# Kernel optimization log

Measured on AMD Instinct MI355X. Metric: run time of the kernel, lower is better.

The kernel has to match this reference:

```python
import jax, jax.numpy as jnp
import numpy as np

MESSAGE_PASSES = 3  # constants.message_passes
F_NODE = 64   # hidden_node_features
F_EDGE = 16   # n_edge_features
M_MSG = 64    # message_size
OUT_DIM = 128
B, N = 8, 256
EDGE_DENSITY = 0.1


def setup_inputs() -> dict:
    key = jax.random.key(0)
    ks = jax.random.split(key, 12)
    nodes = jax.random.normal(ks[0], (B, N, F_NODE), dtype=jnp.float32)
    # sparse positive edge features: rand * bernoulli connectivity (avg degree ~ N*density)
    raw = jax.random.uniform(ks[1], (B, N, N, F_EDGE), dtype=jnp.float32)
    conn = (jax.random.uniform(ks[2], (B, N, N)) < EDGE_DENSITY).astype(jnp.float32)
    edges = raw * conn[..., None]
    s = 0.05
    return {
        "nodes": nodes,
        "edges": edges,
        # message MLP: cat(neighbour, edge) -> message_size
        "W_msg": jax.random.normal(ks[3], (F_NODE + F_EDGE, M_MSG), dtype=jnp.float32) * s,
        "b_msg": jnp.zeros((M_MSG,), dtype=jnp.float32),
        # GRU cell (input=message_size, hidden=F_NODE), gates [r|z|n]
        "W_i": jax.random.normal(ks[4], (M_MSG, 3 * F_NODE), dtype=jnp.float32) * s,
        "W_h": jax.random.normal(ks[5], (F_NODE, 3 * F_NODE), dtype=jnp.float32) * s,
        "b_i": jnp.zeros((3 * F_NODE,), dtype=jnp.float32),
        "b_h": jnp.zeros((3 * F_NODE,), dtype=jnp.float32),
        # gated readout
        "W_g": jax.random.normal(ks[6], (2 * F_NODE, OUT_DIM), dtype=jnp.float32) * s,
        "b_g": jnp.zeros((OUT_DIM,), dtype=jnp.float32),
        "W_e": jax.random.normal(ks[7], (F_NODE, OUT_DIM), dtype=jnp.float32) * s,
        "b_e": jnp.zeros((OUT_DIM,), dtype=jnp.float32),
    }


def reference(nodes, edges, W_msg, b_msg, W_i, W_h, b_i, b_h, W_g, b_g, W_e, b_e):
    # adjacency[b,i,j] != 0  <=>  edge (i<-j) exists (original: edges.sum(3).nonzero)
    adjacency = edges.sum(axis=-1)                                   # (B,N,N)
    nbr_mask = (adjacency != 0).astype(nodes.dtype)                  # (B,N,N)
    node_mask = (adjacency.sum(axis=-1) != 0)                        # (B,N) bool
    node_mask_f = node_mask.astype(nodes.dtype)

    h = nodes                                                        # hidden_nodes init = nodes
    b, n, f = nodes.shape
    for _ in range(MESSAGE_PASSES):
        # message_terms over all (node i, neighbour j) pairs; masked sum == padded-gather sum
        nghb = jnp.broadcast_to(h[:, None, :, :], (b, n, n, f))      # (B,N,N,F) neighbour feats
        feat = jnp.concatenate([nghb, edges], axis=-1)               # (B,N,N,F+E)
        terms = jax.nn.relu(feat @ W_msg + b_msg)                    # (B,N,N,M)
        messages = jnp.einsum('bijm,bij->bim', terms, nbr_mask)      # summation aggregation
        # GRU cell update
        gi = messages @ W_i + b_i                                    # (B,N,3F)
        gh = h @ W_h + b_h
        ir, iz, inn = jnp.split(gi, 3, axis=-1)
        hr, hz, hn = jnp.split(gh, 3, axis=-1)
        r = jax.nn.sigmoid(ir + hr)
        z = jax.nn.sigmoid(iz + hz)
        ng = jnp.tanh(inn + r * hn)
        h_new = (1.0 - z) * ng + z * h
        # only nodes with nonzero degree are scattered back (original indexes node_batch idc)
        h = jnp.where(node_mask[..., None], h_new, h)

    # gated readout: sum_i mask_i * sigmoid(g([h_i, x_i])) * e(h_i)
    gate = jax.nn.sigmoid(jnp.concatenate([h, nodes], axis=-1) @ W_g + b_g)  # (B,N,OUT)
    emb = h @ W_e + b_e                                                      # (B,N,OUT)
    out = jnp.einsum('bno,bn->bo', gate * emb, node_mask_f)                  # (B,OUT)
    return out
```

## Files before the change

### kernel.cpp

```cpp
#include <hip/hip_runtime.h>
#include <hip/hip_bf16.h>

#define BB 8
#define NN 256
#define FF 64
#define EE 16
#define MM 64
#define G3 192
#define OUTD 128
#define ROWS (BB*NN)
#define MAXD 64

__device__ __forceinline__ float sigmoidf_(float x) {
    return 1.0f / (1.0f + __expf(-x));
}

__global__ __launch_bounds__(256) void k_prep(
    const float* __restrict__ nodes, const float* __restrict__ edges,
    const float* __restrict__ Wmsg, const float* __restrict__ bmsg,
    int* __restrict__ deg, int* __restrict__ nbr,
    float* __restrict__ h, float* __restrict__ hn, float* __restrict__ out)
{
    int row = blockIdx.x;
    int tid = threadIdx.x;
    int lane = tid & 63, wv = tid >> 6;
    __shared__ int wcnt[4];
    __shared__ float snode[FF];

    const float4* ep = (const float4*)(edges + (((size_t)row) * NN + tid) * EE);
    float4 a = ep[0], b4 = ep[1], c4 = ep[2], d4 = ep[3];
    float s = a.x+a.y+a.z+a.w + b4.x+b4.y+b4.z+b4.w
            + c4.x+c4.y+c4.z+c4.w + d4.x+d4.y+d4.z+d4.w;
    bool pred = (s != 0.0f);
    unsigned long long m = __ballot(pred);
    if (lane == 0) wcnt[wv] = __popcll(m);
    if (tid < FF) snode[tid] = nodes[(size_t)row * FF + tid];
    __syncthreads();

    int base = 0;
    #pragma unroll
    for (int q = 0; q < 4; ++q) base += (q < wv) ? wcnt[q] : 0;
    int slot = base + __popcll(m & ((1ull << lane) - 1ull));
    if (pred && slot < MAXD) nbr[row * MAXD + slot] = tid;

    if (tid == 0) {
        int tot = wcnt[0] + wcnt[1] + wcnt[2] + wcnt[3];
        deg[row] = (tot < MAXD) ? tot : MAXD;
    }
    if (tid < FF) h[row * FF + tid] = snode[tid];
    if (tid < MM) {
        float acc = bmsg[tid];
        #pragma unroll 8
        for (int k = 0; k < FF; ++k) acc += snode[k] * Wmsg[k * MM + tid];
        hn[row * MM + tid] = acc;
    }
    if (row == 0) {
        #pragma unroll
        for (int i = 0; i < (BB * OUTD) / 256; ++i) out[i * 256 + tid] = 0.0f;
    }
}

__global__ __launch_bounds__(512, 8) void k_pass2(
    const float* __restrict__ edges,
    const float* __restrict__ Wmsg, const float* __restrict__ bmsg,
    const float* __restrict__ Wi, const float* __restrict__ Wh,
    const float* __restrict__ bi, const float* __restrict__ bh,
    const float* __restrict__ nodes,
    const float* __restrict__ Wg, const float* __restrict__ bg,
    const float* __restrict__ We, const float* __restrict__ be,
    const int* __restrict__ deg, const int* __restrict__ nbr,
    const float* __restrict__ hn_in, float* __restrict__ hn_out,
    float* __restrict__ h, float* __restrict__ out, int last)
{
    const int r0  = blockIdx.x * 2;
    const int b   = r0 >> 8;
    const int tid = threadIdx.x;
    const int w   = tid >> 6;
    const int lane = tid & 63;

    __shared__ int   snbr[2][MAXD];
    __shared__ int   sdeg[2];
    __shared__ float efeat[2][MAXD][EE];
    __shared__ float part[8][MM];
    __shared__ float smsg[2][MM];
    __shared__ float shold[2][FF];
    __shared__ float sx[2][FF];
    __shared__ float gI[2][3][FF], gH[2][3][FF];
    __shared__ float shnew[2][FF];
    __shared__ float sg[2][OUTD], se[2][OUTD];

    if (tid < 2) sdeg[tid] = deg[r0 + tid];
    if (tid < 2 * MAXD) {
        int r = tid >> 6;
        snbr[r][tid & 63] = nbr[(r0 + r) * MAXD + (tid & 63)];
    }
    if (tid < 2 * FF) {
        int r = tid >> 6;
        shold[r][tid & 63] = h[(size_t)(r0 + r) * FF + (tid & 63)];
    }
    if (last && tid >= 2 * FF && tid < 4 * FF) {
        int r = (tid >> 6) & 1;
        sx[r][tid & 63] = nodes[(size_t)(r0 + r) * FF + (tid & 63)];
    }

    float we[EE];
    #pragma unroll
    for (int k = 0; k < EE; ++k) we[k] = Wmsg[(FF + k) * MM + lane];
    __syncthreads();

    #pragma unroll
    for (int r = 0; r < 2; ++r) {
        int cnt = sdeg[r] * EE;
        for (int i = tid; i < cnt; i += 512) {
            int slot = i >> 4, k = i & 15;
            efeat[r][slot][k] = edges[(((size_t)(r0 + r)) * NN + snbr[r][slot]) * EE + k];
        }
    }
    __syncthreads();

    {
        int r = w >> 2, sub = w & 3;
        int d = sdeg[r];
        const float* hb = hn_in + (size_t)b * NN * MM;
        float acc = 0.0f;
        for (int s = sub; s < d; s += 4) {
            int j = snbr[r][s];
            float term = hb[j * MM + lane];
            #pragma unroll
            for (int k = 0; k < EE; ++k) term += efeat[r][s][k] * we[k];
            acc += fmaxf(term, 0.0f);
        }
        part[w][lane] = acc;
    }
    __syncthreads();
    if ((w & 3) == 0) {
        int r = w >> 2;
        smsg[r][lane] = part[w][lane] + part[w + 1][lane]
                      + part[w + 2][lane] + part[w + 3][lane];
    }
    __syncthreads();

    if (w < 3) {
        float a0 = bi[w * FF + lane], a1 = a0;
        #pragma unroll 4
        for (int k = 0; k < FF; ++k) {
            float wgt = Wi[k * G3 + w * FF + lane];
            a0 += smsg[0][k] * wgt;
            a1 += smsg[1][k] * wgt;
        }
        gI[0][w][lane] = a0; gI[1][w][lane] = a1;
    } else if (w < 6) {
        int g = w - 3;
        float a0 = bh[g * FF + lane], a1 = a0;
        #pragma unroll 4
        for (int k = 0; k < FF; ++k) {
            float wgt = Wh[k * G3 + g * FF + lane];
            a0 += shold[0][k] * wgt;
            a1 += shold[1][k] * wgt;
        }
        gH[0][g][lane] = a0; gH[1][g][lane] = a1;
    }
    __syncthreads();

    if (tid < 2 * FF) {
        int r = tid >> 6, tt = tid & 63;
        float rr = sigmoidf_(gI[r][0][tt] + gH[r][0][tt]);
        float zz = sigmoidf_(gI[r][1][tt] + gH[r][1][tt]);
        float ng = tanhf(gI[r][2][tt] + rr * gH[r][2][tt]);
        float hold = shold[r][tt];
        float hnew = (1.0f - zz) * ng + zz * hold;
        if (sdeg[r] == 0) hnew = hold;
        shnew[r][tt] = hnew;
        h[(size_t)(r0 + r) * FF + tt] = hnew;
    }
    __syncthreads();

    if (!last) {
        {
            int r = w >> 2, kq = w & 3;
            float p = 0.0f;
            #pragma unroll
            for (int kk = 0; kk < 16; ++kk) {
                int k = kq * 16 + kk;
                p += shnew[r][k] * Wmsg[k * MM + lane];
            }
            part[w][lane] = p;
        }
        __syncthreads();
        if (tid < 2 * MM) {
            int r = tid >> 6, tt = tid & 63;
            hn_out[(size_t)(r0 + r) * MM + tt] = bmsg[tt]
                + part[r*4+0][tt] + part[r*4+1][tt] + part[r*4+2][tt] + part[r*4+3][tt];
        }
    } else {
        int grp = tid >> 7, o = tid & 127;
        int r = grp >> 1, kind = grp & 1;
        if (kind == 0) {
            float g = bg[o];
            #pragma unroll 4
            for (int k = 0; k < FF; ++k) g += shnew[r][k] * Wg[k * OUTD + o];
            #pragma unroll 4
            for (int k = 0; k < FF; ++k) g += sx[r][k] * Wg[(FF + k) * OUTD + o];
            sg[r][o] = g;
        } else {
            float e = be[o];
            #pragma unroll 4
            for (int k = 0; k < FF; ++k) e += shnew[r][k] * We[k * OUTD + o];
            se[r][o] = e;
        }
        __syncthreads();
        if (tid < OUTD) {
            float v0 = (sdeg[0] != 0) ? sigmoidf_(sg[0][tid]) * se[0][tid] : 0.0f;
            float v1 = (sdeg[1] != 0) ? sigmoidf_(sg[1][tid]) * se[1][tid] : 0.0f;
            atomicAdd(&out[b * OUTD + tid], v0 + v1);
        }
    }
}

extern "C" void kernel_launch(void* const* d_in, const int* in_sizes, int n_in,
                              void* d_out, int out_size, void* d_ws, size_t ws_size,
                              hipStream_t stream) {
    const float* nodes = (const float*)d_in[0];
    const float* edges = (const float*)d_in[1];
    const float* Wmsg  = (const float*)d_in[2];
    const float* bmsg  = (const float*)d_in[3];
    const float* Wi    = (const float*)d_in[4];
    const float* Wh    = (const float*)d_in[5];
    const float* bi    = (const float*)d_in[6];
    const float* bh    = (const float*)d_in[7];
    const float* Wg    = (const float*)d_in[8];
    const float* bg    = (const float*)d_in[9];
    const float* We    = (const float*)d_in[10];
    const float* be    = (const float*)d_in[11];
    float* out = (float*)d_out;
    char* ws = (char*)d_ws;

    int*   deg  = (int*)ws;
    int*   nbr  = (int*)(ws + 8192);
    float* h    = (float*)(ws + 8192 + (size_t)ROWS * MAXD * 4);
    float* hnA  = h   + (size_t)ROWS * FF;
    float* hnB  = hnA + (size_t)ROWS * MM;

    k_prep<<<ROWS, 256, 0, stream>>>(nodes, edges, Wmsg, bmsg, deg, nbr, h, hnA, out);

    k_pass2<<<ROWS/2, 512, 0, stream>>>(edges, Wmsg, bmsg, Wi, Wh, bi, bh,
                                        nodes, Wg, bg, We, be, deg, nbr,
                                        hnA, hnB, h, out, 0);
    k_pass2<<<ROWS/2, 512, 0, stream>>>(edges, Wmsg, bmsg, Wi, Wh, bi, bh,
                                        nodes, Wg, bg, We, be, deg, nbr,
                                        hnB, hnA, h, out, 0);
    k_pass2<<<ROWS/2, 512, 0, stream>>>(edges, Wmsg, bmsg, Wi, Wh, bi, bh,
                                        nodes, Wg, bg, We, be, deg, nbr,
                                        hnA, hnB, h, out, 1);
}
```

Measured before the change: 146.7 us.

## Fuse adjacency prep with first message pass and compact edge features

Merges the prep kernel with the first message-passing iteration. Each block now scans edges for two rows, builds the neighbour lists, and writes the nonzero edge features into a compact per-row buffer. It then computes the first pass's messages directly from neighbour node features through the full Wmsg, so no precomputed projection is needed. The later passes read the compact edge-feature buffer with float4 loads instead of gathering from the large dense edges tensor, and the kernel count drops from four to three. In exchange the first pass does more FLOPs per edge and uses a larger shared-memory footprint for Wmsg, which may reduce occupancy.

```diff
diff --git a/kernel.cpp b/kernel.cpp
--- a/kernel.cpp
+++ b/kernel.cpp
@@ -1,5 +1,4 @@
 #include <hip/hip_runtime.h>
-#include <hip/hip_bf16.h>
 
 #define BB 8
 #define NN 256
@@ -15,53 +14,170 @@
     return 1.0f / (1.0f + __expf(-x));
 }
 
-__global__ __launch_bounds__(256) void k_prep(
+__global__ __launch_bounds__(512, 8) void k_p0(
     const float* __restrict__ nodes, const float* __restrict__ edges,
     const float* __restrict__ Wmsg, const float* __restrict__ bmsg,
-    int* __restrict__ deg, int* __restrict__ nbr,
-    float* __restrict__ h, float* __restrict__ hn, float* __restrict__ out)
+    const float* __restrict__ Wi,   const float* __restrict__ Wh,
+    const float* __restrict__ bi,   const float* __restrict__ bh,
+    int* __restrict__ deg, int* __restrict__ nbr, float* __restrict__ gef,
+    float* __restrict__ h, float* __restrict__ hn_out, float* __restrict__ out)
 {
-    int row = blockIdx.x;
-    int tid = threadIdx.x;
-    int lane = tid & 63, wv = tid >> 6;
-    __shared__ int wcnt[4];
-    __shared__ float snode[FF];
-
-    const float4* ep = (const float4*)(edges + (((size_t)row) * NN + tid) * EE);
-    float4 a = ep[0], b4 = ep[1], c4 = ep[2], d4 = ep[3];
-    float s = a.x+a.y+a.z+a.w + b4.x+b4.y+b4.z+b4.w
-            + c4.x+c4.y+c4.z+c4.w + d4.x+d4.y+d4.z+d4.w;
+    const int r0  = blockIdx.x * 2;
+    const int b   = r0 >> 8;
+    const int tid = threadIdx.x;
+    const int w   = tid >> 6;
+    const int lane = tid & 63;
+
+    __shared__ int   snbr[2][MAXD];
+    __shared__ int   sdeg[2];
+    __shared__ int   wcnt[8];
+    __shared__ __align__(16) float efeat[2][MAXD][EE];
+    __shared__ float swm[FF][MM];
+    __shared__ float part[8][MM];
+    __shared__ float smsg[2][MM];
+    __shared__ float shold[2][FF];
+    __shared__ float gI[2][3][FF], gH[2][3][FF];
+
+    if (blockIdx.x == 0) { out[tid] = 0.0f; out[tid + 512] = 0.0f; }
+
+    const int rr0 = tid >> 8;
+    const int j0  = tid & 255;
+    const float4* ep = (const float4*)(edges + (((size_t)(r0 + rr0)) * NN + j0) * EE);
+    float4 ea = ep[0], eb = ep[1], ec = ep[2], ed = ep[3];
+    float s = ea.x+ea.y+ea.z+ea.w + eb.x+eb.y+eb.z+eb.w
+            + ec.x+ec.y+ec.z+ec.w + ed.x+ed.y+ed.z+ed.w;
     bool pred = (s != 0.0f);
     unsigned long long m = __ballot(pred);
-    if (lane == 0) wcnt[wv] = __popcll(m);
-    if (tid < FF) snode[tid] = nodes[(size_t)row * FF + tid];
-    __syncthreads();
-
-    int base = 0;
+    if (lane == 0) wcnt[w] = __popcll(m);
+    if (tid < 2 * FF) {
+        int r = tid >> 6;
+        shold[r][tid & 63] = nodes[(size_t)(r0 + r) * FF + (tid & 63)];
+    }
+    for (int i = tid; i < FF * MM; i += 512) swm[i >> 6][i & 63] = Wmsg[i];
+    __syncthreads();
+
+    {
+        int wb = rr0 * 4, base = 0;
+        #pragma unroll
+        for (int q = 0; q < 4; ++q) base += (wb + q < w) ? wcnt[wb + q] : 0;
+        int slot = base + __popcll(m & ((1ull << lane) - 1ull));
+        if (pred && slot < MAXD) {
+            snbr[rr0][slot] = j0;
+            float4* dl = (float4*)efeat[rr0][slot];
+            dl[0] = ea; dl[1] = eb; dl[2] = ec; dl[3] = ed;
+            nbr[(r0 + rr0) * MAXD + slot] = j0;
+            float4* dg = (float4*)(gef + ((size_t)(r0 + rr0) * MAXD + slot) * EE);
+            dg[0] = ea; dg[1] = eb; dg[2] = ec; dg[3] = ed;
+        }
+    }
+    if (tid == 0) {
+        int t0 = wcnt[0]+wcnt[1]+wcnt[2]+wcnt[3];
+        int t1 = wcnt[4]+wcnt[5]+wcnt[6]+wcnt[7];
+        sdeg[0] = t0 < MAXD ? t0 : MAXD;
+        sdeg[1] = t1 < MAXD ? t1 : MAXD;
+        deg[r0] = sdeg[0]; deg[r0 + 1] = sdeg[1];
+    }
+    float we[EE];
     #pragma unroll
-    for (int q = 0; q < 4; ++q) base += (q < wv) ? wcnt[q] : 0;
-    int slot = base + __popcll(m & ((1ull << lane) - 1ull));
-    if (pred && slot < MAXD) nbr[row * MAXD + slot] = tid;
-
-    if (tid == 0) {
-        int tot = wcnt[0] + wcnt[1] + wcnt[2] + wcnt[3];
-        deg[row] = (tot < MAXD) ? tot : MAXD;
-    }
-    if (tid < FF) h[row * FF + tid] = snode[tid];
-    if (tid < MM) {
-        float acc = bmsg[tid];
-        #pragma unroll 8
-        for (int k = 0; k < FF; ++k) acc += snode[k] * Wmsg[k * MM + tid];
-        hn[row * MM + tid] = acc;
-    }
-    if (row == 0) {
+    for (int k = 0; k < EE; ++k) we[k] = Wmsg[(FF + k) * MM + lane];
+    float bm = bmsg[lane];
+    __syncthreads();
+
+    {
+        int r = w >> 2, sub = w & 3;
+        int d = sdeg[r];
+        const float* nball = nodes + (size_t)b * NN * FF;
+        float acc = 0.0f;
+        for (int s2 = sub; s2 < d; s2 += 8) {
+            int sB = s2 + 4;
+            bool h2 = (sB < d);
+            int jA = snbr[r][s2];
+            int jB = h2 ? snbr[r][sB] : jA;
+            const float4* na = (const float4*)(nball + jA * FF);
+            const float4* nb4 = (const float4*)(nball + jB * FF);
+            float tA = bm, tB = bm;
+            #pragma unroll
+            for (int k = 0; k < EE; ++k) tA += efeat[r][s2][k] * we[k];
+            if (h2) {
+                #pragma unroll
+                for (int k = 0; k < EE; ++k) tB += efeat[r][sB][k] * we[k];
+            }
+            #pragma unroll
+            for (int kq = 0; kq < 16; ++kq) {
+                float4 va = na[kq];
+                float4 vb = nb4[kq];
+                float w0 = swm[4*kq+0][lane], w1 = swm[4*kq+1][lane];
+                float w2 = swm[4*kq+2][lane], w3 = swm[4*kq+3][lane];
+                tA += va.x*w0 + va.y*w1 + va.z*w2 + va.w*w3;
+                tB += vb.x*w0 + vb.y*w1 + vb.z*w2 + vb.w*w3;
+            }
+            acc += fmaxf(tA, 0.0f);
+            if (h2) acc += fmaxf(tB, 0.0f);
+        }
+        part[w][lane] = acc;
+    }
+    __syncthreads();
+    if ((w & 3) == 0) {
+        int r = w >> 2;
+        smsg[r][lane] = part[w][lane] + part[w+1][lane]
+                      + part[w+2][lane] + part[w+3][lane];
+    }
+    __syncthreads();
+
+    if (w < 3) {
+        float a0 = bi[w * FF + lane], a1 = a0;
+        #pragma unroll 4
+        for (int k = 0; k < FF; ++k) {
+            float wgt = Wi[k * G3 + w * FF + lane];
+            a0 += smsg[0][k] * wgt;
+            a1 += smsg[1][k] * wgt;
+        }
+        gI[0][w][lane] = a0; gI[1][w][lane] = a1;
+    } else if (w < 6) {
+        int g = w - 3;
+        float a0 = bh[g * FF + lane], a1 = a0;
+        #pragma unroll 4
+        for (int k = 0; k < FF; ++k) {
+            float wgt = Wh[k * G3 + g * FF + lane];
+            a0 += shold[0][k] * wgt;
+            a1 += shold[1][k] * wgt;
+        }
+        gH[0][g][lane] = a0; gH[1][g][lane] = a1;
+    }
+    __syncthreads();
+
+    if (tid < 2 * FF) {
+        int r = tid >> 6, tt = tid & 63;
+        float rg = sigmoidf_(gI[r][0][tt] + gH[r][0][tt]);
+        float zg = sigmoidf_(gI[r][1][tt] + gH[r][1][tt]);
+        float ng = tanhf(gI[r][2][tt] + rg * gH[r][2][tt]);
+        float hold = shold[r][tt];
+        float hnew = (1.0f - zg) * ng + zg * hold;
+        if (sdeg[r] == 0) hnew = hold;
+        shold[r][tt] = hnew;
+        h[(size_t)(r0 + r) * FF + tt] = hnew;
+    }
+    __syncthreads();
+
+    {
+        int r = w >> 2, kq = w & 3;
+        float p = 0.0f;
         #pragma unroll
-        for (int i = 0; i < (BB * OUTD) / 256; ++i) out[i * 256 + tid] = 0.0f;
+        for (int kk = 0; kk < 16; ++kk) {
+            int k = kq * 16 + kk;
+            p += shold[r][k] * swm[k][lane];
+        }
+        part[w][lane] = p;
+    }
+    __syncthreads();
+    if (tid < 2 * MM) {
+        int r = tid >> 6, tt = tid & 63;
+        hn_out[(size_t)(r0 + r) * MM + tt] = bmsg[tt]
+            + part[r*4+0][tt] + part[r*4+1][tt] + part[r*4+2][tt] + part[r*4+3][tt];
     }
 }
 
-__global__ __launch_bounds__(512, 8) void k_pass2(
-    const float* __restrict__ edges,
+__global__ __launch_bounds__(512, 8) void k_p12(
     const float* __restrict__ Wmsg, const float* __restrict__ bmsg,
     const float* __restrict__ Wi, const float* __restrict__ Wh,
     const float* __restrict__ bi, const float* __restrict__ bh,
@@ -69,6 +185,7 @@
     const float* __restrict__ Wg, const float* __restrict__ bg,
     const float* __restrict__ We, const float* __restrict__ be,
     const int* __restrict__ deg, const int* __restrict__ nbr,
+    const float* __restrict__ gef,
     const float* __restrict__ hn_in, float* __restrict__ hn_out,
     float* __restrict__ h, float* __restrict__ out, int last)
 {
@@ -80,7 +197,7 @@
 
     __shared__ int   snbr[2][MAXD];
     __shared__ int   sdeg[2];
-    __shared__ float efeat[2][MAXD][EE];
+    __shared__ __align__(16) float efeat[2][MAXD][EE];
     __shared__ float part[8][MM];
     __shared__ float smsg[2][MM];
     __shared__ float shold[2][FF];
@@ -89,7 +206,9 @@
     __shared__ float shnew[2][FF];
     __shared__ float sg[2][OUTD], se[2][OUTD];
 
-    if (tid < 2) sdeg[tid] = deg[r0 + tid];
+    const int d0 = deg[r0], d1 = deg[r0 + 1];
+    if (tid == 0) { sdeg[0] = d0; sdeg[1] = d1; }
+
     if (tid < 2 * MAXD) {
         int r = tid >> 6;
         snbr[r][tid & 63] = nbr[(r0 + r) * MAXD + (tid & 63)];
@@ -102,20 +221,15 @@
         int r = (tid >> 6) & 1;
         sx[r][tid & 63] = nodes[(size_t)(r0 + r) * FF + (tid & 63)];
     }
-
+    {
+        const float4* g0 = (const float4*)(gef + (size_t)r0 * MAXD * EE);
+        const float4* g1 = (const float4*)(gef + (size_t)(r0 + 1) * MAXD * EE);
+        for (int i = tid; i < d0 * 4; i += 512) ((float4*)efeat[0])[i] = g0[i];
+        for (int i = tid; i < d1 * 4; i += 512) ((float4*)efeat[1])[i] = g1[i];
+    }
     float we[EE];
     #pragma unroll
     for (int k = 0; k < EE; ++k) we[k] = Wmsg[(FF + k) * MM + lane];
-    __syncthreads();
-
-    #pragma unroll
-    for (int r = 0; r < 2; ++r) {
-        int cnt = sdeg[r] * EE;
-        for (int i = tid; i < cnt; i += 512) {
-            int slot = i >> 4, k = i & 15;
-            efeat[r][slot][k] = edges[(((size_t)(r0 + r)) * NN + snbr[r][slot]) * EE + k];
-        }
-    }
     __syncthreads();
 
     {
@@ -237,19 +351,17 @@
 
     int*   deg  = (int*)ws;
     int*   nbr  = (int*)(ws + 8192);
-    float* h    = (float*)(ws + 8192 + (size_t)ROWS * MAXD * 4);
+    float* gef  = (float*)(ws + 8192 + (size_t)ROWS * MAXD * 4);
+    float* h    = gef + (size_t)ROWS * MAXD * EE;
     float* hnA  = h   + (size_t)ROWS * FF;
     float* hnB  = hnA + (size_t)ROWS * MM;
 
-    k_prep<<<ROWS, 256, 0, stream>>>(nodes, edges, Wmsg, bmsg, deg, nbr, h, hnA, out);
-
-    k_pass2<<<ROWS/2, 512, 0, stream>>>(edges, Wmsg, bmsg, Wi, Wh, bi, bh,
-                                        nodes, Wg, bg, We, be, deg, nbr,
-                                        hnA, hnB, h, out, 0);
-    k_pass2<<<ROWS/2, 512, 0, stream>>>(edges, Wmsg, bmsg, Wi, Wh, bi, bh,
-                                        nodes, Wg, bg, We, be, deg, nbr,
-                                        hnB, hnA, h, out, 0);
-    k_pass2<<<ROWS/2, 512, 0, stream>>>(edges, Wmsg, bmsg, Wi, Wh, bi, bh,
-                                        nodes, Wg, bg, We, be, deg, nbr,
-                                        hnA, hnB, h, out, 1);
+    k_p0<<<ROWS/2, 512, 0, stream>>>(nodes, edges, Wmsg, bmsg, Wi, Wh, bi, bh,
+                                     deg, nbr, gef, h, hnA, out);
+    k_p12<<<ROWS/2, 512, 0, stream>>>(Wmsg, bmsg, Wi, Wh, bi, bh,
+                                      nodes, Wg, bg, We, be, deg, nbr, gef,
+                                      hnA, hnB, h, out, 0);
+    k_p12<<<ROWS/2, 512, 0, stream>>>(Wmsg, bmsg, Wi, Wh, bi, bh,
+                                      nodes, Wg, bg, We, be, deg, nbr, gef,
+                                      hnB, hnA, h, out, 1);
 }
```

Result: slower. 277.6 us (+89.3%).
